# Performance work log

Hardware: AMD Instinct MI355X
Metric: run time of the kernel (lower is better)

Reference implementation:

```python
import jax, jax.numpy as jnp
import numpy as np

N_HEADS = 16
SEG = 64
EPS = 1e-6


def _sigma(x):
    # ELU(x) + 1 kernel feature map (strictly positive)
    return jax.nn.elu(x) + 1.0


def setup_inputs() -> dict:
    key = jax.random.key(0)
    kx, kq, kk, kv, ko = jax.random.split(key, 5)
    B, T, D = 4, 4096, 1024
    scale = D ** -0.5
    return {
        "x": jax.random.normal(kx, (B, T, D), dtype=jnp.float32),
        "W_q": jax.random.normal(kq, (D, D), dtype=jnp.float32) * scale,
        "W_k": jax.random.normal(kk, (D, D), dtype=jnp.float32) * scale,
        "W_v": jax.random.normal(kv, (D, D), dtype=jnp.float32) * scale,
        "W_o": jax.random.normal(ko, (D, D), dtype=jnp.float32) * scale,
        "beta_param": jnp.zeros((N_HEADS,), dtype=jnp.float32),
    }


def _infini_attention(x, W_q, W_k, W_v, W_o, beta_param):
    B, T, D = x.shape
    H = N_HEADS
    dk = D // H
    assert T % SEG == 0
    S = T // SEG

    def proj(W):
        # nn.Linear: x @ W.T ; split heads -> (B,H,T,dk) -> (S,B,H,SEG,dk)
        y = (x @ W.T).reshape(B, T, H, dk).transpose(0, 2, 1, 3)
        return y.reshape(B, H, S, SEG, dk).transpose(2, 0, 1, 3, 4)

    Qs, Ks, Vs = proj(W_q), proj(W_k), proj(W_v)

    beta = jax.nn.sigmoid(beta_param).reshape(1, H, 1, 1)
    causal = jnp.triu(jnp.ones((SEG, SEG), dtype=bool), k=1)
    inv_sqrt_dk = 1.0 / jnp.sqrt(jnp.asarray(dk, x.dtype))

    M0 = jnp.zeros((B, H, dk, dk), dtype=x.dtype)
    z0 = jnp.zeros((B, H, dk), dtype=x.dtype)

    def step(carry, qkv):
        M, z = carry
        q, k, v = qkv  # each (B,H,SEG,dk)
        # Eq.4 memory retrieval
        sq = _sigma(q)
        denom_q = jnp.sum(sq * z[:, :, None, :], axis=-1, keepdims=True) + EPS
        A_mem = jnp.matmul(sq, M) / denom_q
        # local causal softmax attention
        scores = jnp.matmul(q, jnp.swapaxes(k, -2, -1)) * inv_sqrt_dk
        scores = jnp.where(causal, -jnp.inf, scores)
        A_dot = jnp.matmul(jax.nn.softmax(scores, axis=-1), v)
        A_s = beta * A_mem + (1.0 - beta) * A_dot
        # Eq.5 delta-rule memory update
        sk = _sigma(k)
        denom_k = jnp.sum(sk * z[:, :, None, :], axis=-1, keepdims=True) + EPS
        V_prev = jnp.matmul(sk, M) / denom_k
        M_new = M + jnp.einsum("bhtk,bhtv->bhkv", sk, v - V_prev)
        z_new = z + jnp.sum(sk, axis=-2)
        return (M_new, z_new), A_s

    (M, z), outs = jax.lax.scan(step, (M0, z0), (Qs, Ks, Vs))
    # outs: (S,B,H,SEG,dk) -> (B,T,D)
    out = outs.transpose(1, 3, 0, 2, 4).reshape(B, S * SEG, H, dk)
    # careful: need segment-major time ordering -> (B, H, T, dk) then (B,T,H,dk)
    out = outs.transpose(1, 2, 0, 3, 4).reshape(B, H, T, dk)
    out = out.transpose(0, 2, 1, 3).reshape(B, T, D)
    out = out @ W_o.T
    return out, M.mean(0), z.mean(0)


def reference(x, W_q, W_k, W_v, W_o, beta_param):
    return _infini_attention(x, W_q, W_k, W_v, W_o, beta_param)
```

## Files before the change

### kernel.cpp

```cpp
#include <hip/hip_runtime.h>

typedef __bf16 bf16_t;
typedef __bf16 bf16x8 __attribute__((ext_vector_type(8)));
typedef __bf16 bf16x4 __attribute__((ext_vector_type(4)));
typedef float  f32x4  __attribute__((ext_vector_type(4)));

__device__ __forceinline__ void gload16(const bf16_t* g, bf16_t* l) {
    __builtin_amdgcn_global_load_lds(
        (const __attribute__((address_space(1))) void*)(g),
        (__attribute__((address_space(3))) void*)(l), 16, 0, 0);
}

__global__ __launch_bounds__(256) void cast_bf16_kernel(const float* __restrict__ in,
                                                        bf16_t* __restrict__ out, int n4) {
    int i = blockIdx.x * 256 + threadIdx.x;
    if (i >= n4) return;
    f32x4 v = *reinterpret_cast<const f32x4*>(in + (size_t)i * 4);
    bf16x4 o;
    o[0] = (bf16_t)v[0]; o[1] = (bf16_t)v[1]; o[2] = (bf16_t)v[2]; o[3] = (bf16_t)v[3];
    *reinterpret_cast<bf16x4*>(out + (size_t)i * 4) = o;
}

__device__ __forceinline__ bf16x8 sigma8(bf16x8 x) {
    bf16x8 o;
#pragma unroll
    for (int j = 0; j < 8; j++) {
        float f = (float)x[j];
        float sg = f > 0.f ? f + 1.f : __expf(f);
        o[j] = (bf16_t)sg;
    }
    return o;
}

template <int OUT_BF16>
__global__ __launch_bounds__(512, 2) void gemm256(const bf16_t* __restrict__ A,
                                                  const bf16_t* __restrict__ Bm,
                                                  void* __restrict__ Cv,
                                                  int M, int N, int K) {
    __shared__ bf16_t As[4][256 * 32];
    __shared__ bf16_t Bs[4][256 * 32];

    int bid = blockIdx.x;
    int xq = bid & 7, jq = bid >> 3;
    int bm = xq * 8 + (jq >> 2), bn = jq & 3;

    int tid = threadIdx.x;
    int w = tid >> 6, lane = tid & 63;
    int wm = w >> 2, wn = w & 3;
    int lr = lane & 15, lk = lane >> 4;

    int srow = lane >> 2;
    int schunk = (lane & 3) ^ (srow & 3);
    const bf16_t* gA0 = A  + (size_t)(bm * 256 + w * 32 + srow) * K + schunk * 8;
    const bf16_t* gA1 = gA0 + (size_t)16 * K;
    const bf16_t* gB0 = Bm + (size_t)(bn * 256 + w * 32 + srow) * K + schunk * 8;
    const bf16_t* gB1 = gB0 + (size_t)16 * K;
    int lO0 = (w * 32) * 32 + lane * 8;
    int lO1 = (w * 32 + 16) * 32 + lane * 8;

    int chunkb = (lk ^ (lr & 3)) << 4;
    int aoff[8], boff[4];
#pragma unroll
    for (int mi = 0; mi < 8; mi++) aoff[mi] = (wm * 128 + mi * 16 + lr) * 64 + chunkb;
#pragma unroll
    for (int ni = 0; ni < 4; ni++) boff[ni] = (wn * 64 + ni * 16 + lr) * 64 + chunkb;

    f32x4 acc[8][4];
#pragma unroll
    for (int mi = 0; mi < 8; mi++)
#pragma unroll
        for (int ni = 0; ni < 4; ni++) acc[mi][ni] = (f32x4){0.f, 0.f, 0.f, 0.f};

    const int NT = K >> 5;

    auto STAGE = [&](int t) {
        int slot = t & 3;
        size_t ko = (size_t)t * 32;
        gload16(gA0 + ko, &As[slot][lO0]);
        gload16(gA1 + ko, &As[slot][lO1]);
        gload16(gB0 + ko, &Bs[slot][lO0]);
        gload16(gB1 + ko, &Bs[slot][lO1]);
    };

    STAGE(0); STAGE(1); STAGE(2);

#pragma unroll 1
    for (int t = 0; t < NT; ++t) {
        int ahead = NT - 1 - t;
        if (ahead >= 2)      asm volatile("s_waitcnt vmcnt(8)" ::: "memory");
        else if (ahead == 1) asm volatile("s_waitcnt vmcnt(4)" ::: "memory");
        else                 asm volatile("s_waitcnt vmcnt(0)" ::: "memory");
        __builtin_amdgcn_sched_barrier(0);
        __builtin_amdgcn_s_barrier();
        __builtin_amdgcn_sched_barrier(0);

        const char* pa = (const char*)(&As[t & 3][0]);
        const char* pb = (const char*)(&Bs[t & 3][0]);
        bf16x8 af[8], bfr[4];
#pragma unroll
        for (int mi = 0; mi < 8; mi++)
            af[mi] = *reinterpret_cast<const bf16x8*>(pa + aoff[mi]);
#pragma unroll
        for (int ni = 0; ni < 4; ni++)
            bfr[ni] = *reinterpret_cast<const bf16x8*>(pb + boff[ni]);

        if (t + 3 < NT) STAGE(t + 3);

        asm volatile("s_waitcnt lgkmcnt(0)" ::: "memory");
        __builtin_amdgcn_sched_barrier(0);
        __builtin_amdgcn_s_setprio(1);
#pragma unroll
        for (int mi = 0; mi < 8; mi++)
#pragma unroll
            for (int ni = 0; ni < 4; ni++)
                acc[mi][ni] = __builtin_amdgcn_mfma_f32_16x16x32_bf16(af[mi], bfr[ni], acc[mi][ni], 0, 0, 0);
        __builtin_amdgcn_s_setprio(0);
    }

    int row0 = bm * 256 + wm * 128 + lk * 4;
    int col0 = bn * 256 + wn * 64 + lr;
#pragma unroll
    for (int mi = 0; mi < 8; mi++)
#pragma unroll
        for (int ni = 0; ni < 4; ni++)
#pragma unroll
            for (int jj = 0; jj < 4; jj++) {
                size_t idx = (size_t)(row0 + mi * 16 + jj) * N + (col0 + ni * 16);
                float v = acc[mi][ni][jj];
                if (OUT_BF16) reinterpret_cast<bf16_t*>(Cv)[idx] = (bf16_t)v;
                else          reinterpret_cast<float*>(Cv)[idx]  = v;
            }
}

__global__ __launch_bounds__(256) void attn_kernel(const bf16_t* __restrict__ Qb,
                                                   bf16_t* __restrict__ Kb,
                                                   bf16_t* __restrict__ Vb,
                                                   bf16_t* __restrict__ skTg,
                                                   float* __restrict__ csum,
                                                   bf16_t* __restrict__ Adot) {
    __shared__ bf16_t kS[64 * 72];
    __shared__ bf16_t vS[64 * 72];
    __shared__ bf16_t skT[64 * 72];
    __shared__ bf16_t vT[64 * 72];
    __shared__ bf16_t pS[64 * 72];
    __shared__ float  scr[64 * 68];

    int u = blockIdx.x;
    int bh = u >> 6, s = u & 63;
    int b = bh >> 4, h = bh & 15;
    int tid = threadIdx.x;
    int w = tid >> 6, lane = tid & 63;
    int lr = lane & 15, lk = lane >> 4;
    int r = tid >> 2, qd = tid & 3, c0 = qd << 4;

    size_t vseg = ((size_t)b * 4096 + s * 64) * 1024 + (size_t)h * 64;
    size_t sb = ((size_t)bh * 64 + s) * 4096;

    {
        bf16x8 k0 = *reinterpret_cast<const bf16x8*>(Kb + vseg + (size_t)r * 1024 + c0);
        bf16x8 k1 = *reinterpret_cast<const bf16x8*>(Kb + vseg + (size_t)r * 1024 + c0 + 8);
        bf16x8 v0 = *reinterpret_cast<const bf16x8*>(Vb + vseg + (size_t)r * 1024 + c0);
        bf16x8 v1 = *reinterpret_cast<const bf16x8*>(Vb + vseg + (size_t)r * 1024 + c0 + 8);
        *reinterpret_cast<bf16x8*>(&kS[r * 72 + c0])     = k0;
        *reinterpret_cast<bf16x8*>(&kS[r * 72 + c0 + 8]) = k1;
        *reinterpret_cast<bf16x8*>(&vS[r * 72 + c0])     = v0;
        *reinterpret_cast<bf16x8*>(&vS[r * 72 + c0 + 8]) = v1;
        bf16x8 s0 = sigma8(k0), s1 = sigma8(k1);
        *reinterpret_cast<bf16x8*>(Kb + vseg + (size_t)r * 1024 + c0)     = s0;
        *reinterpret_cast<bf16x8*>(Kb + vseg + (size_t)r * 1024 + c0 + 8) = s1;
#pragma unroll
        for (int j = 0; j < 8; j++) {
            skT[(c0 + j) * 72 + r]     = s0[j];
            skT[(c0 + 8 + j) * 72 + r] = s1[j];
            vT[(c0 + j) * 72 + r]      = v0[j];
            vT[(c0 + 8 + j) * 72 + r]  = v1[j];
        }
    }
    __syncthreads();

    if (tid < 64) {
        float acc = 0.f;
#pragma unroll 8
        for (int t = 0; t < 64; t++) acc += (float)skT[tid * 72 + t];
        csum[((size_t)bh * 64 + s) * 64 + tid] = acc;
    }
    *reinterpret_cast<bf16x8*>(skTg + sb + (size_t)r * 64 + c0) =
        *reinterpret_cast<const bf16x8*>(&skT[r * 72 + c0]);
    *reinterpret_cast<bf16x8*>(skTg + sb + (size_t)r * 64 + c0 + 8) =
        *reinterpret_cast<const bf16x8*>(&skT[r * 72 + c0 + 8]);
    *reinterpret_cast<bf16x8*>(Vb + vseg + (size_t)r * 1024 + c0) =
        *reinterpret_cast<const bf16x8*>(&vT[r * 72 + c0]);
    *reinterpret_cast<bf16x8*>(Vb + vseg + (size_t)r * 1024 + c0 + 8) =
        *reinterpret_cast<const bf16x8*>(&vT[r * 72 + c0 + 8]);

    {
        bf16x8 aq[2];
#pragma unroll
        for (int ks = 0; ks < 2; ks++)
            aq[ks] = *reinterpret_cast<const bf16x8*>(Qb + vseg + (size_t)(w * 16 + lr) * 1024 + lk * 8 + ks * 32);
        f32x4 sc[4];
#pragma unroll
        for (int ct = 0; ct < 4; ct++) {
            sc[ct] = (f32x4){0.f, 0.f, 0.f, 0.f};
#pragma unroll
            for (int ks = 0; ks < 2; ks++) {
                bf16x8 bfrag = *reinterpret_cast<const bf16x8*>(&kS[(ct * 16 + lr) * 72 + lk * 8 + ks * 32]);
                sc[ct] = __builtin_amdgcn_mfma_f32_16x16x32_bf16(aq[ks], bfrag, sc[ct], 0, 0, 0);
            }
        }
#pragma unroll
        for (int ct = 0; ct < 4; ct++)
#pragma unroll
            for (int j = 0; j < 4; j++)
                scr[(w * 16 + lk * 4 + j) * 68 + ct * 16 + lr] = sc[ct][j] * 0.125f;
    }
    __syncthreads();

    {
        float p[16];
        float mx = -3.4e38f;
        const float* srow_p = &scr[r * 68 + c0];
#pragma unroll
        for (int i = 0; i < 16; i++) {
            int c = c0 + i;
            float v = (c <= r) ? srow_p[i] : -3.4e38f;
            p[i] = v;
            mx = fmaxf(mx, v);
        }
        mx = fmaxf(mx, __shfl_xor(mx, 1));
        mx = fmaxf(mx, __shfl_xor(mx, 2));
        float sum = 0.f;
#pragma unroll
        for (int i = 0; i < 16; i++) {
            int c = c0 + i;
            float e = (c <= r) ? __expf(p[i] - mx) : 0.f;
            p[i] = e;
            sum += e;
        }
        sum += __shfl_xor(sum, 1);
        sum += __shfl_xor(sum, 2);
        float inv = 1.f / sum;
        bf16x8 p0, p1;
#pragma unroll
        for (int j = 0; j < 8; j++) {
            p0[j] = (bf16_t)(p[j] * inv);
            p1[j] = (bf16_t)(p[8 + j] * inv);
        }
        *reinterpret_cast<bf16x8*>(&pS[r * 72 + c0])     = p0;
        *reinterpret_cast<bf16x8*>(&pS[r * 72 + c0 + 8]) = p1;
    }
    __syncthreads();

    {
        f32x4 ad[4];
#pragma unroll
        for (int ct = 0; ct < 4; ct++) {
            ad[ct] = (f32x4){0.f, 0.f, 0.f, 0.f};
#pragma unroll
            for (int ks = 0; ks < 2; ks++) {
                bf16x8 afrag = *reinterpret_cast<const bf16x8*>(&pS[(w * 16 + lr) * 72 + lk * 8 + ks * 32]);
                bf16x8 bfrag = *reinterpret_cast<const bf16x8*>(&vT[(ct * 16 + lr) * 72 + lk * 8 + ks * 32]);
                ad[ct] = __builtin_amdgcn_mfma_f32_16x16x32_bf16(afrag, bfrag, ad[ct], 0, 0, 0);
            }
        }
#pragma unroll
        for (int ct = 0; ct < 4; ct++)
#pragma unroll
            for (int j = 0; j < 4; j++)
                kS[(w * 16 + lk * 4 + j) * 72 + ct * 16 + lr] = (bf16_t)ad[ct][j];
    }
    __syncthreads();
    *reinterpret_cast<bf16x8*>(Adot + sb + (size_t)r * 64 + c0) =
        *reinterpret_cast<const bf16x8*>(&kS[r * 72 + c0]);
    *reinterpret_cast<bf16x8*>(Adot + sb + (size_t)r * 64 + c0 + 8) =
        *reinterpret_cast<const bf16x8*>(&kS[r * 72 + c0 + 8]);
}

__global__ __launch_bounds__(64) void zprefix_kernel(const float* __restrict__ csum,
                                                     float* __restrict__ zx,
                                                     float* __restrict__ zfin) {
    int bh = blockIdx.x;
    int d = threadIdx.x;
    float z = 0.f;
    for (int s = 0; s < 64; s++) {
        size_t o = ((size_t)bh * 64 + s) * 64 + d;
        zx[o] = z;
        z += csum[o];
    }
    zfin[bh * 64 + d] = z;
}

__global__ __launch_bounds__(128) void denom_kernel(const bf16_t* __restrict__ Qb,
                                                    const bf16_t* __restrict__ sK,
                                                    const float* __restrict__ zx,
                                                    float* __restrict__ invq,
                                                    float* __restrict__ invk) {
    __shared__ float zL[64];
    int u = blockIdx.x;
    int bh = u >> 6, s = u & 63;
    int b = bh >> 4, h = bh & 15;
    int tid = threadIdx.x;
    if (tid < 64) zL[tid] = zx[((size_t)bh * 64 + s) * 64 + tid];
    __syncthreads();
    int row = tid & 63;
    bool isq = tid < 64;
    const bf16_t* src = (isq ? Qb : sK) +
                        ((size_t)b * 4096 + s * 64 + row) * 1024 + (size_t)h * 64;
    float acc = 0.f;
#pragma unroll
    for (int blk = 0; blk < 8; blk++) {
        bf16x8 v = *reinterpret_cast<const bf16x8*>(src + blk * 8);
#pragma unroll
        for (int j = 0; j < 8; j++) {
            float f = (float)v[j];
            float sg;
            if (isq) {
                sg = f > 0.f ? f + 1.f : __expf(f);
                sg = (float)(bf16_t)sg;
            } else {
                sg = f;
            }
            acc = __builtin_fmaf(sg, zL[blk * 8 + j], acc);
        }
    }
    float inv = 1.f / (acc + 1e-6f);
    float* dst = isq ? invq : invk;
    dst[((size_t)bh * 64 + s) * 64 + row] = inv;
}

__global__ __launch_bounds__(64, 1) void scan_kernel(const bf16_t* __restrict__ sK,
                                                     const bf16_t* __restrict__ vTg,
                                                     const bf16_t* __restrict__ skTg,
                                                     const float* __restrict__ invk,
                                                     bf16_t* __restrict__ Msnap,
                                                     float* __restrict__ Mfin) {
    __shared__ bf16_t MbL[16 * 72];
    __shared__ bf16_t uTL[16 * 72];
    __shared__ float  ikL[64];

    int blk = blockIdx.x;
    int bh = blk & 63, cq = blk >> 6;
    int c0 = cq << 4;
    int b = bh >> 4, h = bh & 15;
    int lane = threadIdx.x;
    int lr = lane & 15, lk = lane >> 4;
    int vr = lane >> 2, vt0 = (lane & 3) << 4;

    size_t chbase = ((size_t)b * 4096) * 1024 + (size_t)h * 64;
    size_t stbase = (size_t)bh * 64 * 4096;

    auto swz = [](bf16_t* base, int row, int intra) -> bf16_t* {
        return (bf16_t*)((char*)base + row * 144 + (intra ^ ((row & 7) << 4)));
    };

    for (int i = lane; i < 16 * 72; i += 64) MbL[i] = (bf16_t)0.f;
    f32x4 Mreg[4];
#pragma unroll
    for (int rt = 0; rt < 4; rt++) Mreg[rt] = (f32x4){0.f, 0.f, 0.f, 0.f};

    bf16x8 cK[4][2], cT[4][2];
#pragma unroll
    for (int rt = 0; rt < 4; rt++)
#pragma unroll
        for (int ks = 0; ks < 2; ks++) {
            cK[rt][ks] = *reinterpret_cast<const bf16x8*>(
                sK + chbase + (size_t)(rt * 16 + lr) * 1024 + lk * 8 + ks * 32);
            cT[rt][ks] = *reinterpret_cast<const bf16x8*>(
                skTg + stbase + (size_t)(rt * 16 + lr) * 64 + lk * 8 + ks * 32);
        }
    {
        bf16x8 v0 = *reinterpret_cast<const bf16x8*>(vTg + chbase + (size_t)(c0 + vr) * 1024 + vt0);
        bf16x8 v1 = *reinterpret_cast<const bf16x8*>(vTg + chbase + (size_t)(c0 + vr) * 1024 + vt0 + 8);
        *reinterpret_cast<bf16x8*>(swz(uTL, vr, vt0 * 2))      = v0;
        *reinterpret_cast<bf16x8*>(swz(uTL, vr, vt0 * 2 + 16)) = v1;
        ikL[lane] = invk[(size_t)bh * 4096 + lane];
    }

    for (int s = 0; s < 64; s++) {
        bf16x8 nK[4][2], nT[4][2], nv0, nv1;
        float nik = 0.f;
        if (s < 63) {
            size_t vs2 = chbase + (size_t)(s + 1) * 65536;
            size_t sb2 = stbase + (size_t)(s + 1) * 4096;
#pragma unroll
            for (int rt = 0; rt < 4; rt++)
#pragma unroll
                for (int ks = 0; ks < 2; ks++) {
                    nK[rt][ks] = *reinterpret_cast<const bf16x8*>(
                        sK + vs2 + (size_t)(rt * 16 + lr) * 1024 + lk * 8 + ks * 32);
                    nT[rt][ks] = *reinterpret_cast<const bf16x8*>(
                        skTg + sb2 + (size_t)(rt * 16 + lr) * 64 + lk * 8 + ks * 32);
                }
            nv0 = *reinterpret_cast<const bf16x8*>(vTg + vs2 + (size_t)(c0 + vr) * 1024 + vt0);
            nv1 = *reinterpret_cast<const bf16x8*>(vTg + vs2 + (size_t)(c0 + vr) * 1024 + vt0 + 8);
            nik = invk[(size_t)bh * 4096 + (size_t)(s + 1) * 64 + lane];
        }

        bf16x8 mb0 = *reinterpret_cast<const bf16x8*>(swz(MbL, lr, lk * 16));
        bf16x8 mb1 = *reinterpret_cast<const bf16x8*>(swz(MbL, lr, lk * 16 + 64));
        f32x4 Y[4];
#pragma unroll
        for (int rt = 0; rt < 4; rt++) {
            Y[rt] = (f32x4){0.f, 0.f, 0.f, 0.f};
            Y[rt] = __builtin_amdgcn_mfma_f32_16x16x32_bf16(cK[rt][0], mb0, Y[rt], 0, 0, 0);
            Y[rt] = __builtin_amdgcn_mfma_f32_16x16x32_bf16(cK[rt][1], mb1, Y[rt], 0, 0, 0);
        }

#pragma unroll
        for (int rt = 0; rt < 4; rt++) {
            bf16x4 vv = *reinterpret_cast<const bf16x4*>(swz(uTL, lr, rt * 32 + lk * 8));
            bf16x4 uu;
#pragma unroll
            for (int j = 0; j < 4; j++) {
                float ik = ikL[rt * 16 + lk * 4 + j];
                uu[j] = (bf16_t)((float)vv[j] - Y[rt][j] * ik);
            }
            *reinterpret_cast<bf16x4*>(swz(uTL, lr, rt * 32 + lk * 8)) = uu;
        }

        bf16x8 ub0 = *reinterpret_cast<const bf16x8*>(swz(uTL, lr, lk * 16));
        bf16x8 ub1 = *reinterpret_cast<const bf16x8*>(swz(uTL, lr, lk * 16 + 64));
#pragma unroll
        for (int rt = 0; rt < 4; rt++) {
            Mreg[rt] = __builtin_amdgcn_mfma_f32_16x16x32_bf16(cT[rt][0], ub0, Mreg[rt], 0, 0, 0);
            Mreg[rt] = __builtin_amdgcn_mfma_f32_16x16x32_bf16(cT[rt][1], ub1, Mreg[rt], 0, 0, 0);
        }

#pragma unroll
        for (int rt = 0; rt < 4; rt++) {
            bf16x4 mp;
#pragma unroll
            for (int j = 0; j < 4; j++) mp[j] = (bf16_t)Mreg[rt][j];
            *reinterpret_cast<bf16x4*>(swz(MbL, lr, rt * 32 + lk * 8)) = mp;
            if (s < 63)
                *reinterpret_cast<bf16x4*>(
                    Msnap + (((size_t)bh * 64 + s + 1) * 64 + c0 + lr) * 64 + rt * 16 + lk * 4) = mp;
        }

        if (s < 63) {
#pragma unroll
            for (int rt = 0; rt < 4; rt++)
#pragma unroll
                for (int ks = 0; ks < 2; ks++) { cK[rt][ks] = nK[rt][ks]; cT[rt][ks] = nT[rt][ks]; }
            *reinterpret_cast<bf16x8*>(swz(uTL, vr, vt0 * 2))      = nv0;
            *reinterpret_cast<bf16x8*>(swz(uTL, vr, vt0 * 2 + 16)) = nv1;
            ikL[lane] = nik;
        }
    }

#pragma unroll
    for (int rt = 0; rt < 4; rt++)
#pragma unroll
        for (int j = 0; j < 4; j++)
            Mfin[(size_t)bh * 4096 + (size_t)(rt * 16 + lk * 4 + j) * 64 + c0 + lr] = Mreg[rt][j];
}

__global__ __launch_bounds__(256) void combine_kernel(const bf16_t* __restrict__ Qb,
                                                      const bf16_t* __restrict__ Msnap,
                                                      const bf16_t* __restrict__ Adot,
                                                      const float* __restrict__ invq,
                                                      const float* __restrict__ beta_param,
                                                      bf16_t* __restrict__ Op) {
    __shared__ bf16_t oS[64 * 72];
    __shared__ bf16_t adS[64 * 72];
    __shared__ float  iq[64];

    int u = blockIdx.x;
    int bh = u >> 6, s = u & 63;
    int b = bh >> 4, h = bh & 15;
    int tid = threadIdx.x;
    int w = tid >> 6, lane = tid & 63;
    int lr = lane & 15, lk = lane >> 4;
    int r = tid >> 2, c0 = (tid & 3) << 4;

    size_t vseg = ((size_t)b * 4096 + s * 64) * 1024 + (size_t)h * 64;
    size_t sb = ((size_t)bh * 64 + s) * 4096;
    size_t ib = ((size_t)bh * 64 + s) * 64;

    float beta = 1.f / (1.f + __expf(-beta_param[h]));
    float omb = 1.f - beta;

    *reinterpret_cast<bf16x8*>(&adS[r * 72 + c0]) =
        *reinterpret_cast<const bf16x8*>(Adot + sb + (size_t)r * 64 + c0);
    *reinterpret_cast<bf16x8*>(&adS[r * 72 + c0 + 8]) =
        *reinterpret_cast<const bf16x8*>(Adot + sb + (size_t)r * 64 + c0 + 8);
    if (tid < 64) iq[tid] = invq[ib + tid];

    f32x4 Y[4];
#pragma unroll
    for (int ct = 0; ct < 4; ct++) Y[ct] = (f32x4){0.f, 0.f, 0.f, 0.f};
    if (s > 0) {
        bf16x8 aq[2];
#pragma unroll
        for (int ks = 0; ks < 2; ks++)
            aq[ks] = sigma8(*reinterpret_cast<const bf16x8*>(
                Qb + vseg + (size_t)(w * 16 + lr) * 1024 + lk * 8 + ks * 32));
#pragma unroll
        for (int ct = 0; ct < 4; ct++)
#pragma unroll
            for (int ks = 0; ks < 2; ks++) {
                bf16x8 bfrag = *reinterpret_cast<const bf16x8*>(
                    Msnap + sb + (size_t)(ct * 16 + lr) * 64 + lk * 8 + ks * 32);
                Y[ct] = __builtin_amdgcn_mfma_f32_16x16x32_bf16(aq[ks], bfrag, Y[ct], 0, 0, 0);
            }
    }
    __syncthreads();

#pragma unroll
    for (int ct = 0; ct < 4; ct++) {
        int colc = ct * 16 + lr;
#pragma unroll
        for (int j = 0; j < 4; j++) {
            int t = w * 16 + lk * 4 + j;
            float o = beta * (Y[ct][j] * iq[t]) + omb * (float)adS[t * 72 + colc];
            oS[t * 72 + colc] = (bf16_t)o;
        }
    }
    __syncthreads();

    *reinterpret_cast<bf16x8*>(Op + vseg + (size_t)r * 1024 + c0) =
        *reinterpret_cast<const bf16x8*>(&oS[r * 72 + c0]);
    *reinterpret_cast<bf16x8*>(Op + vseg + (size_t)r * 1024 + c0 + 8) =
        *reinterpret_cast<const bf16x8*>(&oS[r * 72 + c0 + 8]);
}

__global__ __launch_bounds__(256) void mean_kernel(const float* __restrict__ Mfin,
                                                   const float* __restrict__ zfin,
                                                   float* __restrict__ out) {
    int idx = blockIdx.x * 256 + threadIdx.x;
    if (idx < 65536) {
        out[16777216 + idx] = 0.25f * (Mfin[idx] + Mfin[idx + 65536] +
                                       Mfin[idx + 131072] + Mfin[idx + 196608]);
    } else if (idx < 66560) {
        int j = idx - 65536;
        out[16842752 + j] = 0.25f * (zfin[j] + zfin[j + 1024] + zfin[j + 2048] + zfin[j + 3072]);
    }
}

extern "C" void kernel_launch(void* const* d_in, const int* in_sizes, int n_in,
                              void* d_out, int out_size, void* d_ws, size_t ws_size,
                              hipStream_t stream) {
    const float* x      = (const float*)d_in[0];
    const float* Wq     = (const float*)d_in[1];
    const float* Wk     = (const float*)d_in[2];
    const float* Wv     = (const float*)d_in[3];
    const float* Wo     = (const float*)d_in[4];
    const float* beta_p = (const float*)d_in[5];
    float* out = (float*)d_out;
    char* ws = (char*)d_ws;

    const size_t NX = 16777216ull;
    const size_t NW = 1048576ull;

    bf16_t* xb   = (bf16_t*)ws;
    bf16_t* Adot = xb;
    bf16_t* Wqb  = (bf16_t*)(ws + 33554432);
    bf16_t* Wkb  = (bf16_t*)(ws + 35651584);
    bf16_t* Wvb  = (bf16_t*)(ws + 37748736);
    bf16_t* Wob  = (bf16_t*)(ws + 39845888);
    bf16_t* Qb   = (bf16_t*)(ws + 41943040);
    bf16_t* Kb   = (bf16_t*)(ws + 75497472);
    bf16_t* Vb   = (bf16_t*)(ws + 109051904);
    bf16_t* skT  = (bf16_t*)(ws + 142606336);
    bf16_t* Op   = (bf16_t*)(ws + 176160768);
    float*  csum = (float*)(ws + 209715200);
    float*  zx   = (float*)(ws + 210763776);
    float*  invq = (float*)(ws + 211812352);
    float*  invk = (float*)(ws + 212860928);
    float*  Mfin = (float*)(ws + 213909504);
    float*  zfin = (float*)(ws + 214958080);
    bf16_t* Msnap = (bf16_t*)d_out;

    cast_bf16_kernel<<<dim3(16384), dim3(256), 0, stream>>>(x, xb, (int)(NX / 4));
    cast_bf16_kernel<<<dim3(1024), dim3(256), 0, stream>>>(Wq, Wqb, (int)(NW / 4));
    cast_bf16_kernel<<<dim3(1024), dim3(256), 0, stream>>>(Wk, Wkb, (int)(NW / 4));
    cast_bf16_kernel<<<dim3(1024), dim3(256), 0, stream>>>(Wv, Wvb, (int)(NW / 4));
    cast_bf16_kernel<<<dim3(1024), dim3(256), 0, stream>>>(Wo, Wob, (int)(NW / 4));

    gemm256<1><<<dim3(256), dim3(512), 0, stream>>>(xb, Wqb, (void*)Qb, 16384, 1024, 1024);
    gemm256<1><<<dim3(256), dim3(512), 0, stream>>>(xb, Wkb, (void*)Kb, 16384, 1024, 1024);
    gemm256<1><<<dim3(256), dim3(512), 0, stream>>>(xb, Wvb, (void*)Vb, 16384, 1024, 1024);

    attn_kernel<<<dim3(4096), dim3(256), 0, stream>>>(Qb, Kb, Vb, skT, csum, Adot);
    zprefix_kernel<<<dim3(64), dim3(64), 0, stream>>>(csum, zx, zfin);
    denom_kernel<<<dim3(4096), dim3(128), 0, stream>>>(Qb, Kb, zx, invq, invk);
    scan_kernel<<<dim3(256), dim3(64), 0, stream>>>(Kb, Vb, skT, invk, Msnap, Mfin);
    combine_kernel<<<dim3(4096), dim3(256), 0, stream>>>(Qb, Msnap, Adot, invq, beta_p, Op);

    gemm256<0><<<dim3(256), dim3(512), 0, stream>>>(Op, Wob, d_out, 16384, 1024, 1024);
    mean_kernel<<<dim3(260), dim3(256), 0, stream>>>(Mfin, zfin, out);
}
```

Baseline: 347.2 us.

## Merge weight casts, change GEMM LDS swizzle, prefetch zprefix loads

Replaces the four separate weight-cast launches with one kernel that picks its matrix by block index, removing three launches. Changes the XOR swizzle in the GEMM's LDS staging and fragment reads from row bits 0-1 to row bits 1-2, aiming to reduce LDS bank conflicts. In zprefix, the 64 csum loads are issued up front into registers so the serial prefix loop no longer waits on each load, at the cost of more registers.

```diff
diff --git a/kernel.cpp b/kernel.cpp
--- a/kernel.cpp
+++ b/kernel.cpp
@@ -21,6 +21,24 @@
     *reinterpret_cast<bf16x4*>(out + (size_t)i * 4) = o;
 }
 
+__global__ __launch_bounds__(256) void cast4_kernel(const float* __restrict__ w0,
+                                                    const float* __restrict__ w1,
+                                                    const float* __restrict__ w2,
+                                                    const float* __restrict__ w3,
+                                                    bf16_t* __restrict__ o0,
+                                                    bf16_t* __restrict__ o1,
+                                                    bf16_t* __restrict__ o2,
+                                                    bf16_t* __restrict__ o3) {
+    int which = blockIdx.x >> 10;
+    int i = (blockIdx.x & 1023) * 256 + threadIdx.x;
+    const float* in = (which == 0) ? w0 : (which == 1) ? w1 : (which == 2) ? w2 : w3;
+    bf16_t*     out = (which == 0) ? o0 : (which == 1) ? o1 : (which == 2) ? o2 : o3;
+    f32x4 v = *reinterpret_cast<const f32x4*>(in + (size_t)i * 4);
+    bf16x4 o;
+    o[0] = (bf16_t)v[0]; o[1] = (bf16_t)v[1]; o[2] = (bf16_t)v[2]; o[3] = (bf16_t)v[3];
+    *reinterpret_cast<bf16x4*>(out + (size_t)i * 4) = o;
+}
+
 __device__ __forceinline__ bf16x8 sigma8(bf16x8 x) {
     bf16x8 o;
 #pragma unroll
@@ -50,7 +68,7 @@
     int lr = lane & 15, lk = lane >> 4;
 
     int srow = lane >> 2;
-    int schunk = (lane & 3) ^ (srow & 3);
+    int schunk = (lane & 3) ^ ((lane >> 3) & 3);
     const bf16_t* gA0 = A  + (size_t)(bm * 256 + w * 32 + srow) * K + schunk * 8;
     const bf16_t* gA1 = gA0 + (size_t)16 * K;
     const bf16_t* gB0 = Bm + (size_t)(bn * 256 + w * 32 + srow) * K + schunk * 8;
@@ -58,7 +76,7 @@
     int lO0 = (w * 32) * 32 + lane * 8;
     int lO1 = (w * 32 + 16) * 32 + lane * 8;
 
-    int chunkb = (lk ^ (lr & 3)) << 4;
+    int chunkb = (lk ^ ((lr >> 1) & 3)) << 4;
     int aoff[8], boff[4];
 #pragma unroll
     for (int mi = 0; mi < 8; mi++) aoff[mi] = (wm * 128 + mi * 16 + lr) * 64 + chunkb;
@@ -281,11 +299,15 @@
                                                      float* __restrict__ zfin) {
     int bh = blockIdx.x;
     int d = threadIdx.x;
+    float c[64];
+#pragma unroll
+    for (int s = 0; s < 64; s++)
+        c[s] = csum[((size_t)bh * 64 + s) * 64 + d];
     float z = 0.f;
+#pragma unroll
     for (int s = 0; s < 64; s++) {
-        size_t o = ((size_t)bh * 64 + s) * 64 + d;
-        zx[o] = z;
-        z += csum[o];
+        zx[((size_t)bh * 64 + s) * 64 + d] = z;
+        z += c[s];
     }
     zfin[bh * 64 + d] = z;
 }
@@ -550,7 +572,6 @@
     char* ws = (char*)d_ws;
 
     const size_t NX = 16777216ull;
-    const size_t NW = 1048576ull;
 
     bf16_t* xb   = (bf16_t*)ws;
     bf16_t* Adot = xb;
@@ -572,10 +593,7 @@
     bf16_t* Msnap = (bf16_t*)d_out;
 
     cast_bf16_kernel<<<dim3(16384), dim3(256), 0, stream>>>(x, xb, (int)(NX / 4));
-    cast_bf16_kernel<<<dim3(1024), dim3(256), 0, stream>>>(Wq, Wqb, (int)(NW / 4));
-    cast_bf16_kernel<<<dim3(1024), dim3(256), 0, stream>>>(Wk, Wkb, (int)(NW / 4));
-    cast_bf16_kernel<<<dim3(1024), dim3(256), 0, stream>>>(Wv, Wvb, (int)(NW / 4));
-    cast_bf16_kernel<<<dim3(1024), dim3(256), 0, stream>>>(Wo, Wob, (int)(NW / 4));
+    cast4_kernel<<<dim3(4096), dim3(256), 0, stream>>>(Wq, Wk, Wv, Wo, Wqb, Wkb, Wvb, Wob);
 
     gemm256<1><<<dim3(256), dim3(512), 0, stream>>>(xb, Wqb, (void*)Qb, 16384, 1024, 1024);
     gemm256<1><<<dim3(256), dim3(512), 0, stream>>>(xb, Wkb, (void*)Kb, 16384, 1024, 1024);
```

New measurement: 335.9 us. -3.2%, faster.
